# Kernel tuning notes

Measured on AMD Instinct MI355X. Metric: run time of the kernel, lower is better.

## Reference

```python
import jax, jax.numpy as jnp
import numpy as np

N_NODES = 50000
N_EDGES = 800000
N_GRAPHS = 512
F_IN = 9
U = 64  # model_units


def _add_self_loops(edge_index, n):
    loop = jnp.arange(n, dtype=edge_index.dtype)
    return jnp.concatenate([edge_index, jnp.stack([loop, loop])], axis=1)


def gat_conv(x, edge_index, W, a_src, a_dst, b):
    # PyG GATConv, heads=1, negative_slope=0.2, add_self_loops=True
    n = x.shape[0]
    ei = _add_self_loops(edge_index, n)
    src, dst = ei[0], ei[1]
    h = x @ W                              # [n, U]
    alpha_s = h @ a_src                    # [n]
    alpha_d = h @ a_dst                    # [n]
    e = jax.nn.leaky_relu(alpha_s[src] + alpha_d[dst], 0.2)   # [E+n]
    m = jax.ops.segment_max(e, dst, num_segments=n)           # stable softmax over incoming edges
    ex = jnp.exp(e - m[dst])
    denom = jax.ops.segment_sum(ex, dst, num_segments=n)
    coef = ex / denom[dst]                 # [E+n]
    out = jax.ops.segment_sum(h[src] * coef[:, None], dst, num_segments=n)
    return out + b


def gcn_conv(x, edge_index, W, b):
    # PyG GCNConv with symmetric normalization and self loops
    n = x.shape[0]
    ei = _add_self_loops(edge_index, n)
    src, dst = ei[0], ei[1]
    h = x @ W                              # [n, U]
    deg = jax.ops.segment_sum(jnp.ones(src.shape, h.dtype), dst, num_segments=n)
    dinv = jnp.where(deg > 0, jax.lax.rsqrt(deg), 0.0)
    norm = dinv[src] * dinv[dst]           # [E+n]
    out = jax.ops.segment_sum(h[src] * norm[:, None], dst, num_segments=n)
    return out + b


def _branch(x, edge_index, W_gat, a_src, a_dst, b_gat, W_gcn, b_gcn, W1, b1, W2, b2, W3, b3):
    x = jnp.tanh(gat_conv(x, edge_index, W_gat, a_src, a_dst, b_gat))
    for i in range(W_gcn.shape[0]):        # model_layers - 1 = 2 GCN layers
        x = jnp.tanh(gcn_conv(x, edge_index, W_gcn[i], b_gcn[i]))
        # dropout is a no-op in eval mode
    x = jnp.tanh(x @ W1 + b1)
    x = jnp.tanh(x @ W2 + b2)
    x = x @ W3 + b3                        # [n, 1]; dropout no-op in eval
    return x


def _mean_pool(x, batch, num_graphs):
    sums = jax.ops.segment_sum(x, batch, num_segments=num_graphs)
    cnt = jax.ops.segment_sum(jnp.ones((x.shape[0],), x.dtype), batch, num_segments=num_graphs)
    return sums / jnp.maximum(cnt, 1.0)[:, None]


def setup_inputs() -> dict:
    key = jax.random.key(0)
    ks = jax.random.split(key, 16)
    inp = {
        "x_a": jax.random.normal(ks[0], (N_NODES, F_IN), jnp.float32),
        "x_b": jax.random.normal(ks[1], (N_NODES, F_IN), jnp.float32),
        "edge_index_a": jax.random.randint(ks[2], (2, N_EDGES), 0, N_NODES, jnp.int32),
        "edge_index_b": jax.random.randint(ks[3], (2, N_EDGES), 0, N_NODES, jnp.int32),
        "batch_a": jnp.sort(jax.random.randint(ks[4], (N_NODES,), 0, N_GRAPHS, jnp.int32)),
        "batch_b": jnp.sort(jax.random.randint(ks[5], (N_NODES,), 0, N_GRAPHS, jnp.int32)),
        # parameters
        "W_gat": jax.random.normal(ks[6], (F_IN, U), jnp.float32) * 0.3,
        "a_src": jax.random.normal(ks[7], (U,), jnp.float32) * 0.3,
        "a_dst": jax.random.normal(ks[8], (U,), jnp.float32) * 0.3,
        "b_gat": jnp.zeros((U,), jnp.float32),
        "W_gcn": jax.random.normal(ks[9], (2, U, U), jnp.float32) * (1.0 / np.sqrt(U)),
        "b_gcn": jnp.zeros((2, U), jnp.float32),
        "W1": jax.random.normal(ks[10], (U, U), jnp.float32) * (1.0 / np.sqrt(U)),
        "b1": jnp.zeros((U,), jnp.float32),
        "W2": jax.random.normal(ks[11], (U, 32), jnp.float32) * (1.0 / np.sqrt(U)),
        "b2": jnp.zeros((32,), jnp.float32),
        "W3": jax.random.normal(ks[12], (32, 1), jnp.float32) * (1.0 / np.sqrt(32.0)),
        "b3": jnp.zeros((1,), jnp.float32),
    }
    return inp


def reference(x_a, x_b, edge_index_a, edge_index_b, batch_a, batch_b,
              W_gat, a_src, a_dst, b_gat, W_gcn, b_gcn, W1, b1, W2, b2, W3, b3):
    params = (W_gat, a_src, a_dst, b_gat, W_gcn, b_gcn, W1, b1, W2, b2, W3, b3)
    ha = _branch(x_a, edge_index_a, *params)
    hb = _branch(x_b, edge_index_b, *params)
    ua = _mean_pool(ha, batch_a, N_GRAPHS)   # [G, 1]
    ub = _mean_pool(hb, batch_b, N_GRAPHS)
    return jax.nn.sigmoid(ub - ua)
```

## Files before the change

kernel.cpp:

```cpp
#include <hip/hip_runtime.h>
#include <hip/hip_fp16.h>
#include <math.h>

#define NN 50000
#define NE 800000
#define NG 512
#define NET (NE + NN)
#define NT2 ((2 * NN + 63) / 64)
#define GN4 ((2 * NN + 3) / 4)
#define TS 72
#define HOFF ((size_t)2 * NN * 32)
#define GXB 391
#define GX (8 * GXB)

#define SLICE 512
#define NSL ((NN + SLICE - 1) / SLICE)
#define CHK 4096
#define NCK ((NET + CHK - 1) / CHK)
#define CAP 10240

typedef unsigned short u16;
typedef _Float16 h8 __attribute__((ext_vector_type(8)));
typedef float f32x4 __attribute__((ext_vector_type(4)));

__device__ __forceinline__ float wsum64(float v) {
#pragma unroll
    for (int o = 32; o > 0; o >>= 1) v += __shfl_down(v, o, 64);
    return v;
}

__device__ __forceinline__ float fast_tanh(float x) {
    return 1.f - 2.f / (__expf(2.f * x) + 1.f);
}


__global__ __launch_bounds__(256) void k_hist(const int* __restrict__ eia,
                                              const int* __restrict__ eib,
                                              int* __restrict__ cnts) {
    __shared__ int h[NSL];
    int b = blockIdx.x;
    int br = b >= NCK, c = b - (br ? NCK : 0);
    int t = threadIdx.x;
    for (int i = t; i < NSL; i += 256) h[i] = 0;
    __syncthreads();
    const int* ei = br ? eib : eia;
    int e0 = c * CHK, e1 = e0 + CHK; if (e1 > NET) e1 = NET;
    for (int e = e0 + t; e < e1; e += 256) {
        int d = (e < NE) ? __builtin_nontemporal_load(&ei[NE + e]) : (e - NE);
        atomicAdd(&h[d >> 9], 1);
    }
    __syncthreads();
    for (int i = t; i < NSL; i += 256) cnts[(br * NSL + i) * NCK + c] = h[i];
}

__global__ __launch_bounds__(64) void k_off1(int* __restrict__ cnts,
                                             int* __restrict__ sliceBase) {
    int b = blockIdx.x;
    int br = b >= NSL, s = b - (br ? NSL : 0);
    int lane = threadIdx.x;
    int* row = cnts + (br * NSL + s) * NCK;
    int run = 0;
    for (int c0 = 0; c0 < NCK; c0 += 64) {
        int c = c0 + lane;
        int v = (c < NCK) ? row[c] : 0;
        int orig = v;
#pragma unroll
        for (int o = 1; o < 64; o <<= 1) {
            int tv = __shfl_up(v, o, 64);
            if (lane >= o) v += tv;
        }
        if (c < NCK) row[c] = run + v - orig;
        run += __shfl(v, 63, 64);
    }
    if (lane == 0) sliceBase[br * (NSL + 1) + s] = run;
}

__global__ void k_off2(int* __restrict__ sliceBase, int* __restrict__ rowptr2,
                       float* __restrict__ pool) {
    int t = threadIdx.x;
    for (int i = t; i < 4 * NG; i += 256) pool[i] = 0.f;
    if (t < 2) {
        int* sb = sliceBase + t * (NSL + 1);
        int run = 0;
        for (int s = 0; s < NSL; s++) { int v = sb[s]; sb[s] = run; run += v; }
        sb[NSL] = run;
        rowptr2[t * (NN + 1) + NN] = run;
    }
}

__global__ __launch_bounds__(256) void k_bucket(const int* __restrict__ eia,
                                                const int* __restrict__ eib,
                                                const int* __restrict__ cnts,
                                                const int* __restrict__ sliceBase,
                                                unsigned int* __restrict__ staging) {
    __shared__ int cur[NSL];
    int b = blockIdx.x;
    int br = b >= NCK, c = b - (br ? NCK : 0);
    int t = threadIdx.x;
    for (int i = t; i < NSL; i += 256)
        cur[i] = cnts[(br * NSL + i) * NCK + c] + sliceBase[br * (NSL + 1) + i];
    __syncthreads();
    const int* ei = br ? eib : eia;
    unsigned int* stg = staging + (size_t)br * NET;
    int e0 = c * CHK, e1 = e0 + CHK; if (e1 > NET) e1 = NET;
    for (int e = e0 + t; e < e1; e += 256) {
        int d, s;
        if (e < NE) {
            d = __builtin_nontemporal_load(&ei[NE + e]);
            s = __builtin_nontemporal_load(&ei[e]);
        } else { d = e - NE; s = d; }
        int pos = atomicAdd(&cur[d >> 9], 1);
        stg[pos] = ((unsigned int)(d & 511) << 16) | (unsigned int)s;
    }
}

__global__ __launch_bounds__(512) void k_slice(const unsigned int* __restrict__ staging,
                                               const int* __restrict__ sliceBase,
                                               int* __restrict__ rowptr2,
                                               float* __restrict__ dinv2,
                                               u16* __restrict__ csr2) {
    __shared__ int sc[512];
    __shared__ int cur[512];
    __shared__ u16 buf[CAP];
    int b = blockIdx.x;
    int br = b >= NSL, sl = b - (br ? NSL : 0);
    int t = threadIdx.x;
    const int* sb = sliceBase + br * (NSL + 1);
    int base = sb[sl], m = sb[sl + 1] - base;
    const unsigned int* st = staging + (size_t)br * NET + base;
    cur[t] = 0;
    __syncthreads();
    for (int i = t; i < m; i += 512) atomicAdd(&cur[st[i] >> 16], 1);
    __syncthreads();
    int v = cur[t];
    sc[t] = v;
    __syncthreads();
    for (int o = 1; o < 512; o <<= 1) {
        int add = (t >= o) ? sc[t - o] : 0;
        __syncthreads();
        sc[t] += add;
        __syncthreads();
    }
    int excl = sc[t] - v;
    int node = sl * SLICE + t;
    if (node < NN) {
        rowptr2[br * (NN + 1) + node] = base + excl;
        dinv2[br * NN + node] = v > 0 ? rsqrtf((float)v) : 0.f;
    }
    cur[t] = excl;
    __syncthreads();
    for (int i = t; i < m; i += 512) {
        unsigned int e = st[i];
        int pos = atomicAdd(&cur[e >> 16], 1);
        if (pos < CAP) buf[pos] = (u16)(e & 0xffffu);
    }
    __syncthreads();
    u16* out = csr2 + (size_t)br * NET + base;
    int mm = m < CAP ? m : CAP;
    for (int i = t; i < mm; i += 512) out[i] = buf[i];
}

__global__ __launch_bounds__(256) void k_wprep(const float* __restrict__ W1,
                                               const float* __restrict__ W2,
                                               const float* __restrict__ Wgcn,
                                               __half* __restrict__ out) {
    int i = blockIdx.x * 256 + threadIdx.x;
    float v;
    if (i < 4096)       { int n = i >> 6,        k = i & 63; v = W1[k * 64 + n]; }
    else if (i < 6144)  { int j = i - 4096; int n = j >> 6, k = j & 63; v = W2[k * 32 + n]; }
    else if (i < 10240) { int j = i - 6144; int n = j >> 6, k = j & 63; v = Wgcn[k * 64 + n]; }
    else                { int j = i - 10240; int n = j >> 6, k = j & 63; v = Wgcn[4096 + k * 64 + n]; }
    out[i] = __float2half(v);
}


__global__ void k_gat_input(const float* __restrict__ xa, const float* __restrict__ xb,
                            const float* __restrict__ Wg,
                            const float* __restrict__ avs, const float* __restrict__ avd,
                            __half* __restrict__ A, float* __restrict__ als,
                            float* __restrict__ ald) {
    __shared__ float sW[9 * 64];
    __shared__ float sas[64], sad[64];
    int t = threadIdx.x;
    for (int i = t; i < 9 * 64; i += 256) sW[i] = Wg[i];
    if (t < 64) { sas[t] = avs[t]; sad[t] = avd[t]; }
    __syncthreads();
    int n = blockIdx.x * 4 + (t >> 6);
    int u = t & 63;
    if (n >= 2 * NN) return;
    const float* xp = (n < NN) ? &xa[(size_t)n * 9] : &xb[(size_t)(n - NN) * 9];
    float h = 0.f;
#pragma unroll
    for (int f = 0; f < 9; f++) h += xp[f] * sW[f * 64 + u];
    A[(size_t)(u >> 5) * HOFF + (size_t)n * 32 + (u & 31)] = __float2half(h);
    float ps = wsum64(h * sas[u]);
    float pd = wsum64(h * sad[u]);
    if (u == 0) { als[n] = ps; ald[n] = pd; }
}

__device__ __forceinline__ void fma8(float* acc, float4 f, float w) {
    const __half2* h = (const __half2*)&f;
#pragma unroll
    for (int p = 0; p < 4; p++) {
        float2 v = __half22float2(h[p]);
        acc[2 * p]     += v.x * w;
        acc[2 * p + 1] += v.y * w;
    }
}

__global__ __launch_bounds__(256) void k_gat_gather(
        const int* __restrict__ rowptr2, const u16* __restrict__ csr2,
        const float* __restrict__ als, const float* __restrict__ ald,
        const __half* __restrict__ A, const float* __restrict__ bias,
        __half* __restrict__ B) {
    int bid = blockIdx.x;
    int br = (bid >> 2) & 1;
    int h = (bid >> 1) & 1;
    int k = ((bid >> 3) << 1) + (bid & 1);
    int t = threadIdx.x;
    int lane = t & 63;
    int grp = lane >> 2, li = lane & 3;
    int d = k * 64 + ((t >> 6) << 4) + grp;
    if (d >= NN) return;
    int dg = br * NN + d;
    const int* rp = rowptr2 + br * (NN + 1);
    const u16* cs = csr2 + br * NET;
    int nb = br * NN;
    int beg = rp[d], end = rp[d + 1];
    float ad = ald[dg];
    const float4* Af = (const float4*)A + (size_t)h * 2 * NN * 4;
    float acc[8];
#pragma unroll
    for (int q = 0; q < 8; q++) acc[q] = 0.f;
    float den = 0.f;
    for (int j = beg; j < end; j += 4) {
        int i1 = j + 1, i2 = j + 2, i3 = j + 3;
        int c1 = i1 < end ? i1 : end - 1;
        int c2 = i2 < end ? i2 : end - 1;
        int c3 = i3 < end ? i3 : end - 1;
        int s0 = nb + cs[j];
        int s1 = nb + cs[c1];
        int s2 = nb + cs[c2];
        int s3 = nb + cs[c3];
        float v0 = als[s0] + ad;
        float v1 = als[s1] + ad;
        float v2 = als[s2] + ad;
        float v3 = als[s3] + ad;
        float w0 = __expf(fmaxf(v0, 0.2f * v0));
        float w1 = i1 < end ? __expf(fmaxf(v1, 0.2f * v1)) : 0.f;
        float w2 = i2 < end ? __expf(fmaxf(v2, 0.2f * v2)) : 0.f;
        float w3 = i3 < end ? __expf(fmaxf(v3, 0.2f * v3)) : 0.f;
        den += (w0 + w1) + (w2 + w3);
        float4 f0 = Af[(size_t)s0 * 4 + li];
        float4 f1 = Af[(size_t)s1 * 4 + li];
        float4 f2 = Af[(size_t)s2 * 4 + li];
        float4 f3 = Af[(size_t)s3 * 4 + li];
        fma8(acc, f0, w0);
        fma8(acc, f1, w1);
        fma8(acc, f2, w2);
        fma8(acc, f3, w3);
    }
    float inv = 1.f / den;
    const float4* bf = (const float4*)bias;
    float4 b0 = bf[h * 8 + li * 2], b1 = bf[h * 8 + li * 2 + 1];
    __half2 o[4];
    o[0] = __floats2half2_rn(fast_tanh(acc[0] * inv + b0.x), fast_tanh(acc[1] * inv + b0.y));
    o[1] = __floats2half2_rn(fast_tanh(acc[2] * inv + b0.z), fast_tanh(acc[3] * inv + b0.w));
    o[2] = __floats2half2_rn(fast_tanh(acc[4] * inv + b1.x), fast_tanh(acc[5] * inv + b1.y));
    o[3] = __floats2half2_rn(fast_tanh(acc[6] * inv + b1.z), fast_tanh(acc[7] * inv + b1.w));
    ((float4*)B)[(size_t)h * 2 * NN * 4 + (size_t)dg * 4 + li] = *(float4*)o;
}

__global__ __launch_bounds__(256) void k_gcn_gather(
        const int* __restrict__ rowptr2, const u16* __restrict__ csr2,
        const float* __restrict__ dinv, const __half* __restrict__ Y,
        const float* __restrict__ bias, __half* __restrict__ Bout) {
    int bid = blockIdx.x;
    int br = (bid >> 2) & 1;
    int h = (bid >> 1) & 1;
    int k = ((bid >> 3) << 1) + (bid & 1);
    int t = threadIdx.x;
    int lane = t & 63;
    int grp = lane >> 2, li = lane & 3;
    int d = k * 64 + ((t >> 6) << 4) + grp;
    if (d >= NN) return;
    int dg = br * NN + d;
    const int* rp = rowptr2 + br * (NN + 1);
    const u16* cs = csr2 + br * NET;
    int nb = br * NN;
    int beg = rp[d], end = rp[d + 1];
    const float4* Yf = (const float4*)Y + (size_t)h * 2 * NN * 4;
    float acc[8];
#pragma unroll
    for (int q = 0; q < 8; q++) acc[q] = 0.f;
    for (int j = beg; j < end; j += 4) {
        int i1 = j + 1, i2 = j + 2, i3 = j + 3;
        int c1 = i1 < end ? i1 : end - 1;
        int c2 = i2 < end ? i2 : end - 1;
        int c3 = i3 < end ? i3 : end - 1;
        float w1 = i1 < end ? 1.f : 0.f;
        float w2 = i2 < end ? 1.f : 0.f;
        float w3 = i3 < end ? 1.f : 0.f;
        int s0 = nb + cs[j];
        int s1 = nb + cs[c1];
        int s2 = nb + cs[c2];
        int s3 = nb + cs[c3];
        float4 f0 = Yf[(size_t)s0 * 4 + li];
        float4 f1 = Yf[(size_t)s1 * 4 + li];
        float4 f2 = Yf[(size_t)s2 * 4 + li];
        float4 f3 = Yf[(size_t)s3 * 4 + li];
        fma8(acc, f0, 1.f);
        fma8(acc, f1, w1);
        fma8(acc, f2, w2);
        fma8(acc, f3, w3);
    }
    float dv = dinv[dg];
    const float4* bf = (const float4*)bias;
    float4 b0 = bf[h * 8 + li * 2], b1 = bf[h * 8 + li * 2 + 1];
    __half2 o[4];
    o[0] = __floats2half2_rn(fast_tanh(acc[0] * dv + b0.x), fast_tanh(acc[1] * dv + b0.y));
    o[1] = __floats2half2_rn(fast_tanh(acc[2] * dv + b0.z), fast_tanh(acc[3] * dv + b0.w));
    o[2] = __floats2half2_rn(fast_tanh(acc[4] * dv + b1.x), fast_tanh(acc[5] * dv + b1.y));
    o[3] = __floats2half2_rn(fast_tanh(acc[6] * dv + b1.z), fast_tanh(acc[7] * dv + b1.w));
    ((float4*)Bout)[(size_t)h * 2 * NN * 4 + (size_t)dg * 4 + li] = *(float4*)o;
}

__device__ __forceinline__ void stage_split(const __half* __restrict__ X, int base,
                                            __half* sX, int t) {
    const float4* Xf = (const float4*)X;
#pragma unroll
    for (int rep = 0; rep < 2; rep++) {
        int i = t + rep * 256;
        int row = i >> 3, q = i & 7;
        int h = q >> 2, q2 = q & 3;
        float4 x;
        if (base + row < 2 * NN) x = Xf[(size_t)h * 2 * NN * 4 + (size_t)(base + row) * 4 + q2];
        else x = make_float4(0.f, 0.f, 0.f, 0.f);
        *(float4*)&sX[row * TS + q * 8] = x;
    }
}

__global__ __launch_bounds__(256) void k_lin_tile(
        const __half* __restrict__ X, const __half* __restrict__ Wt,
        const float* __restrict__ dinv, __half* __restrict__ Y) {
    __shared__ __half sX[64 * TS];
    __shared__ __half sW[64 * TS];
    int t = threadIdx.x;
    int base = blockIdx.x * 64;
    const float4* Wf = (const float4*)Wt;
#pragma unroll
    for (int rep = 0; rep < 2; rep++) {
        int i = t + rep * 256;
        int row = i >> 3, q = i & 7;
        *(float4*)&sW[row * TS + q * 8] = Wf[i];
    }
    stage_split(X, base, sX, t);
    __syncthreads();
    int l = t & 63, w = t >> 6;
    int lr = l & 15, lg = l >> 4;
    h8 av0 = *(const h8*)&sX[(16 * w + lr) * TS + 8 * lg];
    h8 av1 = *(const h8*)&sX[(16 * w + lr) * TS + 32 + 8 * lg];
    f32x4 acc[4];
#pragma unroll
    for (int s = 0; s < 4; s++) {
        h8 bv0 = *(const h8*)&sW[(16 * s + lr) * TS + 8 * lg];
        h8 bv1 = *(const h8*)&sW[(16 * s + lr) * TS + 32 + 8 * lg];
        f32x4 c = {0.f, 0.f, 0.f, 0.f};
        c = __builtin_amdgcn_mfma_f32_16x16x32_f16(av0, bv0, c, 0, 0, 0);
        c = __builtin_amdgcn_mfma_f32_16x16x32_f16(av1, bv1, c, 0, 0, 0);
        acc[s] = c;
    }
    int nrow = base + 16 * w + 4 * lg;
    float4 dv4 = *(const float4*)&dinv[16 * w + 4 * lg + base];
#pragma unroll
    for (int s = 0; s < 4; s++) {
        int col = 16 * s + lr;
        size_t cbase = (size_t)(col >> 5) * HOFF + (col & 31);
#pragma unroll
        for (int i = 0; i < 4; i++) {
            int n = nrow + i;
            if (n < 2 * NN) Y[cbase + (size_t)n * 32] = __float2half(acc[s][i] * dv4[i]);
        }
    }
}

__global__ __launch_bounds__(256) void k_mlp_pool(
        const __half* __restrict__ X,
        const int* __restrict__ batch_a, const int* __restrict__ batch_b,
        const __half* __restrict__ W1t, const float* __restrict__ b1,
        const __half* __restrict__ W2t, const float* __restrict__ b2,
        const float* __restrict__ W3, const float* __restrict__ b3,
        float* __restrict__ pool) {
    __shared__ __half sX[64 * TS];
    __shared__ __half sW1[64 * TS];
    __shared__ __half sW2[32 * TS];
    __shared__ float sP[64];
    __shared__ int sKey[64];
    __shared__ float sVal[64];
    int t = threadIdx.x;
    int base = blockIdx.x * 64;
    const float4* W1f = (const float4*)W1t;
    const float4* W2f = (const float4*)W2t;
#pragma unroll
    for (int rep = 0; rep < 2; rep++) {
        int i = t + rep * 256;
        int row = i >> 3, q = i & 7;
        *(float4*)&sW1[row * TS + q * 8] = W1f[i];
    }
    {
        int row = t >> 3, q = t & 7;
        *(float4*)&sW2[row * TS + q * 8] = W2f[t];
    }
    stage_split(X, base, sX, t);
    float bb3 = b3[0];
    __syncthreads();
    int l = t & 63, w = t >> 6;
    int lr = l & 15, lg = l >> 4;
    h8 av0 = *(const h8*)&sX[(16 * w + lr) * TS + 8 * lg];
    h8 av1 = *(const h8*)&sX[(16 * w + lr) * TS + 32 + 8 * lg];
    f32x4 d1[4];
#pragma unroll
    for (int s = 0; s < 4; s++) {
        float bias = b1[16 * s + lr];
        f32x4 c = {bias, bias, bias, bias};
        h8 bv0 = *(const h8*)&sW1[(16 * s + lr) * TS + 8 * lg];
        h8 bv1 = *(const h8*)&sW1[(16 * s + lr) * TS + 32 + 8 * lg];
        c = __builtin_amdgcn_mfma_f32_16x16x32_f16(av0, bv0, c, 0, 0, 0);
        c = __builtin_amdgcn_mfma_f32_16x16x32_f16(av1, bv1, c, 0, 0, 0);
        d1[s] = c;
    }
#pragma unroll
    for (int s = 0; s < 4; s++) {
#pragma unroll
        for (int i = 0; i < 4; i++) {
            sX[(16 * w + 4 * lg + i) * TS + 16 * s + lr] = __float2half(fast_tanh(d1[s][i]));
        }
    }
    __syncthreads();
    h8 a20 = *(const h8*)&sX[(16 * w + lr) * TS + 8 * lg];
    h8 a21 = *(const h8*)&sX[(16 * w + lr) * TS + 32 + 8 * lg];
    f32x4 d2[2];
#pragma unroll
    for (int s = 0; s < 2; s++) {
        float bias = b2[16 * s + lr];
        f32x4 c = {bias, bias, bias, bias};
        h8 bv0 = *(const h8*)&sW2[(16 * s + lr) * TS + 8 * lg];
        h8 bv1 = *(const h8*)&sW2[(16 * s + lr) * TS + 32 + 8 * lg];
        c = __builtin_amdgcn_mfma_f32_16x16x32_f16(a20, bv0, c, 0, 0, 0);
        c = __builtin_amdgcn_mfma_f32_16x16x32_f16(a21, bv1, c, 0, 0, 0);
        d2[s] = c;
    }
    float w3a = W3[lr], w3b = W3[16 + lr];
    float pr[4];
#pragma unroll
    for (int i = 0; i < 4; i++)
        pr[i] = fast_tanh(d2[0][i]) * w3a + fast_tanh(d2[1][i]) * w3b;
#pragma unroll
    for (int o = 1; o < 16; o <<= 1) {
#pragma unroll
        for (int i = 0; i < 4; i++) pr[i] += __shfl_xor(pr[i], o, 16);
    }
    if (lr == 0) {
#pragma unroll
        for (int i = 0; i < 4; i++) sP[16 * w + 4 * lg + i] = pr[i];
    }
    __syncthreads();
    if (t < 64) {
        int n = base + t;
        bool valid = n < 2 * NN;
        int br = n >= NN;
        int g = valid ? (br ? batch_b[n - NN] : batch_a[n]) : -1;
        int key = valid ? (br * 4096 + g) : -1;
        sKey[t] = key;
        sVal[t] = sP[t] + bb3;
        __builtin_amdgcn_s_barrier();
        if (valid && (t == 0 || sKey[t - 1] != key)) {
            float sum = 0.f;
            int cnt = 0;
            for (int j = t; j < 64 && sKey[j] == key; j++) { sum += sVal[j]; cnt++; }
            float* bin = pool + br * 2 * NG;
            atomicAdd(&bin[g], sum);
            atomicAdd(&bin[NG + g], (float)cnt);
        }
    }
}

__global__ void k_final(const float* __restrict__ pool, float* __restrict__ out) {
    int g = blockIdx.x * 256 + threadIdx.x;
    if (g >= NG) return;
    float ua = pool[g] / fmaxf(pool[NG + g], 1.f);
    float ub = pool[2 * NG + g] / fmaxf(pool[3 * NG + g], 1.f);
    float z = ub - ua;
    out[g] = 1.f / (1.f + __expf(-z));
}

extern "C" void kernel_launch(void* const* d_in, const int* in_sizes, int n_in,
                              void* d_out, int out_size, void* d_ws, size_t ws_size,
                              hipStream_t stream) {
    const float* x_a = (const float*)d_in[0];
    const float* x_b = (const float*)d_in[1];
    const int* ei_a = (const int*)d_in[2];
    const int* ei_b = (const int*)d_in[3];
    const int* batch_a = (const int*)d_in[4];
    const int* batch_b = (const int*)d_in[5];
    const float* Wg   = (const float*)d_in[6];
    const float* avs  = (const float*)d_in[7];
    const float* avd  = (const float*)d_in[8];
    const float* bg   = (const float*)d_in[9];
    const float* Wgcn = (const float*)d_in[10];
    const float* bgcn = (const float*)d_in[11];
    const float* W1 = (const float*)d_in[12];
    const float* b1 = (const float*)d_in[13];
    const float* W2 = (const float*)d_in[14];
    const float* b2 = (const float*)d_in[15];
    const float* W3 = (const float*)d_in[16];
    const float* b3 = (const float*)d_in[17];

    char* w = (char*)d_ws;
    __half* A2 = (__half*)w;          w += (size_t)2 * NN * 64 * 2;
    __half* B2 = (__half*)w;          w += (size_t)2 * NN * 64 * 2;
    float* als2 = (float*)w;          w += (size_t)2 * NN * 4;
    float* ald2 = (float*)w;          w += (size_t)2 * NN * 4;
    float* dinv2 = (float*)w;         w += (size_t)2 * NN * 4;
    float* pool = (float*)w;          w += (size_t)4 * NG * 4;
    int* rowptr2 = (int*)w;           w += (size_t)2 * (NN + 1) * 4;
    int* cnts = (int*)w;              w += (size_t)2 * NSL * NCK * 4;
    int* sliceBase = (int*)w;         w += (size_t)2 * (NSL + 1) * 4;
    u16* csr2 = (u16*)w;              w += (size_t)2 * NET * 2;
    __half* wcache = (__half*)w;      w += (size_t)14336 * 2;
    unsigned int* staging = (unsigned int*)A2;

    __half* W1t = wcache;
    __half* W2t = wcache + 4096;
    __half* Wg0t = wcache + 6144;
    __half* Wg1t = wcache + 10240;

    dim3 blk(256);

    k_hist<<<2 * NCK, blk, 0, stream>>>(ei_a, ei_b, cnts);
    k_wprep<<<56, blk, 0, stream>>>(W1, W2, Wgcn, wcache);
    k_off1<<<2 * NSL, dim3(64), 0, stream>>>(cnts, sliceBase);
    k_off2<<<1, blk, 0, stream>>>(sliceBase, rowptr2, pool);
    k_bucket<<<2 * NCK, blk, 0, stream>>>(ei_a, ei_b, cnts, sliceBase, staging);
    k_slice<<<2 * NSL, dim3(512), 0, stream>>>(staging, sliceBase, rowptr2, dinv2, csr2);

    k_gat_input<<<GN4, blk, 0, stream>>>(x_a, x_b, Wg, avs, avd, A2, als2, ald2);
    k_gat_gather<<<GX, blk, 0, stream>>>(rowptr2, csr2, als2, ald2, A2, bg, B2);
    k_lin_tile<<<NT2, blk, 0, stream>>>(B2, Wg0t, dinv2, A2);
    k_gcn_gather<<<GX, blk, 0, stream>>>(rowptr2, csr2, dinv2, A2, bgcn, B2);
    k_lin_tile<<<NT2, blk, 0, stream>>>(B2, Wg1t, dinv2, A2);
    k_gcn_gather<<<GX, blk, 0, stream>>>(rowptr2, csr2, dinv2, A2, bgcn + 64, B2);
    k_mlp_pool<<<NT2, blk, 0, stream>>>(B2, batch_a, batch_b, W1t, b1, W2t, b2, W3, b3, pool);

    k_final<<<(NG + 255) / 256, blk, 0, stream>>>(pool, (float*)d_out);
}
```

Before: 304.9 us.

## Sort destination nodes by in-degree within slices to balance gather wavefronts

k_slice now counting-sorts the nodes of each 512-node slice by in-degree (capped at 63) and writes a permutation array. The GAT and GCN gather kernels read that permutation to pick their destination node, so the 16 nodes sharing a wavefront have similar edge counts and lanes diverge less in the edge loop. In exchange there is an extra indirect load per node, scattered output writes, and padding entries that must be skipped with a guard. Neighbouring nodes in a wavefront are also no longer contiguous, which can hurt locality.

```diff
diff --git a/kernel.cpp b/kernel.cpp
--- a/kernel.cpp
+++ b/kernel.cpp
@@ -10,14 +10,15 @@
 #define GN4 ((2 * NN + 3) / 4)
 #define TS 72
 #define HOFF ((size_t)2 * NN * 32)
-#define GXB 391
-#define GX (8 * GXB)
 
 #define SLICE 512
 #define NSL ((NN + SLICE - 1) / SLICE)
 #define CHK 4096
 #define NCK ((NET + CHK - 1) / CHK)
 #define CAP 10240
+#define NPW (NSL * SLICE)
+
+#define GX (8 * 392)
 
 typedef unsigned short u16;
 typedef _Float16 h8 __attribute__((ext_vector_type(8)));
@@ -118,10 +119,12 @@
                                                const int* __restrict__ sliceBase,
                                                int* __restrict__ rowptr2,
                                                float* __restrict__ dinv2,
-                                               u16* __restrict__ csr2) {
+                                               u16* __restrict__ csr2,
+                                               int* __restrict__ dperm) {
     __shared__ int sc[512];
     __shared__ int cur[512];
     __shared__ u16 buf[CAP];
+    __shared__ int dh[64], dcur[64];
     int b = blockIdx.x;
     int br = b >= NSL, sl = b - (br ? NSL : 0);
     int t = threadIdx.x;
@@ -129,6 +132,7 @@
     int base = sb[sl], m = sb[sl + 1] - base;
     const unsigned int* st = staging + (size_t)br * NET + base;
     cur[t] = 0;
+    if (t < 64) dh[t] = 0;
     __syncthreads();
     for (int i = t; i < m; i += 512) atomicAdd(&cur[st[i] >> 16], 1);
     __syncthreads();
@@ -158,6 +162,21 @@
     u16* out = csr2 + (size_t)br * NET + base;
     int mm = m < CAP ? m : CAP;
     for (int i = t; i < mm; i += 512) out[i] = buf[i];
+    int key = v < 63 ? v : 63;
+    atomicAdd(&dh[key], 1);
+    __syncthreads();
+    if (t < 64) {
+        int x = dh[t], orig = x;
+#pragma unroll
+        for (int o = 1; o < 64; o <<= 1) {
+            int y = __shfl_up(x, o, 64);
+            if (t >= o) x += y;
+        }
+        dcur[t] = x - orig;
+    }
+    __syncthreads();
+    int pos = atomicAdd(&dcur[key], 1);
+    dperm[br * NPW + sl * SLICE + pos] = node;
 }
 
 __global__ __launch_bounds__(256) void k_wprep(const float* __restrict__ W1,
@@ -210,6 +229,7 @@
 
 __global__ __launch_bounds__(256) void k_gat_gather(
         const int* __restrict__ rowptr2, const u16* __restrict__ csr2,
+        const int* __restrict__ dperm,
         const float* __restrict__ als, const float* __restrict__ ald,
         const __half* __restrict__ A, const float* __restrict__ bias,
         __half* __restrict__ B) {
@@ -220,14 +240,16 @@
     int t = threadIdx.x;
     int lane = t & 63;
     int grp = lane >> 2, li = lane & 3;
-    int d = k * 64 + ((t >> 6) << 4) + grp;
-    if (d >= NN) return;
+    int pos = k * 64 + ((t >> 6) << 4) + grp;
+    int d = dperm[br * NPW + pos];
+    bool ok = d < NN;
     int dg = br * NN + d;
     const int* rp = rowptr2 + br * (NN + 1);
     const u16* cs = csr2 + br * NET;
     int nb = br * NN;
-    int beg = rp[d], end = rp[d + 1];
-    float ad = ald[dg];
+    int beg = 0, end = 0;
+    float ad = 0.f;
+    if (ok) { beg = rp[d]; end = rp[d + 1]; ad = ald[dg]; }
     const float4* Af = (const float4*)A + (size_t)h * 2 * NN * 4;
     float acc[8];
 #pragma unroll
@@ -260,6 +282,7 @@
         fma8(acc, f2, w2);
         fma8(acc, f3, w3);
     }
+    if (!ok) return;
     float inv = 1.f / den;
     const float4* bf = (const float4*)bias;
     float4 b0 = bf[h * 8 + li * 2], b1 = bf[h * 8 + li * 2 + 1];
@@ -273,6 +296,7 @@
 
 __global__ __launch_bounds__(256) void k_gcn_gather(
         const int* __restrict__ rowptr2, const u16* __restrict__ csr2,
+        const int* __restrict__ dperm,
         const float* __restrict__ dinv, const __half* __restrict__ Y,
         const float* __restrict__ bias, __half* __restrict__ Bout) {
     int bid = blockIdx.x;
@@ -282,13 +306,15 @@
     int t = threadIdx.x;
     int lane = t & 63;
     int grp = lane >> 2, li = lane & 3;
-    int d = k * 64 + ((t >> 6) << 4) + grp;
-    if (d >= NN) return;
+    int pos = k * 64 + ((t >> 6) << 4) + grp;
+    int d = dperm[br * NPW + pos];
+    bool ok = d < NN;
     int dg = br * NN + d;
     const int* rp = rowptr2 + br * (NN + 1);
     const u16* cs = csr2 + br * NET;
     int nb = br * NN;
-    int beg = rp[d], end = rp[d + 1];
+    int beg = 0, end = 0;
+    if (ok) { beg = rp[d]; end = rp[d + 1]; }
     const float4* Yf = (const float4*)Y + (size_t)h * 2 * NN * 4;
     float acc[8];
 #pragma unroll
@@ -314,6 +340,7 @@
         fma8(acc, f2, w2);
         fma8(acc, f3, w3);
     }
+    if (!ok) return;
     float dv = dinv[dg];
     const float4* bf = (const float4*)bias;
     float4 b0 = bf[h * 8 + li * 2], b1 = bf[h * 8 + li * 2 + 1];
@@ -526,6 +553,7 @@
     int* rowptr2 = (int*)w;           w += (size_t)2 * (NN + 1) * 4;
     int* cnts = (int*)w;              w += (size_t)2 * NSL * NCK * 4;
     int* sliceBase = (int*)w;         w += (size_t)2 * (NSL + 1) * 4;
+    int* dperm = (int*)w;             w += (size_t)2 * NPW * 4;
     u16* csr2 = (u16*)w;              w += (size_t)2 * NET * 2;
     __half* wcache = (__half*)w;      w += (size_t)14336 * 2;
     unsigned int* staging = (unsigned int*)A2;
@@ -542,14 +570,14 @@
     k_off1<<<2 * NSL, dim3(64), 0, stream>>>(cnts, sliceBase);
     k_off2<<<1, blk, 0, stream>>>(sliceBase, rowptr2, pool);
     k_bucket<<<2 * NCK, blk, 0, stream>>>(ei_a, ei_b, cnts, sliceBase, staging);
-    k_slice<<<2 * NSL, dim3(512), 0, stream>>>(staging, sliceBase, rowptr2, dinv2, csr2);
+    k_slice<<<2 * NSL, dim3(512), 0, stream>>>(staging, sliceBase, rowptr2, dinv2, csr2, dperm);
 
     k_gat_input<<<GN4, blk, 0, stream>>>(x_a, x_b, Wg, avs, avd, A2, als2, ald2);
-    k_gat_gather<<<GX, blk, 0, stream>>>(rowptr2, csr2, als2, ald2, A2, bg, B2);
+    k_gat_gather<<<GX, blk, 0, stream>>>(rowptr2, csr2, dperm, als2, ald2, A2, bg, B2);
     k_lin_tile<<<NT2, blk, 0, stream>>>(B2, Wg0t, dinv2, A2);
-    k_gcn_gather<<<GX, blk, 0, stream>>>(rowptr2, csr2, dinv2, A2, bgcn, B2);
+    k_gcn_gather<<<GX, blk, 0, stream>>>(rowptr2, csr2, dperm, dinv2, A2, bgcn, B2);
     k_lin_tile<<<NT2, blk, 0, stream>>>(B2, Wg1t, dinv2, A2);
-    k_gcn_gather<<<GX, blk, 0, stream>>>(rowptr2, csr2, dinv2, A2, bgcn + 64, B2);
+    k_gcn_gather<<<GX, blk, 0, stream>>>(rowptr2, csr2, dperm, dinv2, A2, bgcn + 64, B2);
     k_mlp_pool<<<NT2, blk, 0, stream>>>(B2, batch_a, batch_b, W1t, b1, W2t, b2, W3, b3, pool);
 
     k_final<<<(NG + 255) / 256, blk, 0, stream>>>(pool, (float*)d_out);
```

Result: slower. 339.6 us (+11.4%).
